# Kernel optimization log

Hardware: AMD Instinct MI355X
Metric: run time of the kernel (lower is better)

Reference implementation:

```python
import jax, jax.numpy as jnp
import numpy as np

TEMP = 0.1
EPS = 1e-12  # torch F.normalize eps


def _normalize(v):
    return v / jnp.maximum(jnp.linalg.norm(v, axis=1, keepdims=True), EPS)


def _scale_loss(a1, a2, b1, c1):
    # diag of exp(a1 @ a2.T / temp): computed directly from paired rows
    # (same math as eye-mask + row-sum in the original).
    diag = jnp.exp(jnp.sum(a1 * a2, axis=1) / TEMP)            # [B]
    denom = (jnp.exp(a1 @ b1.T / TEMP).sum(1, keepdims=True)
             + jnp.exp(a1 @ c1.T / TEMP).sum(1, keepdims=True))  # [B,1]
    # NOTE: [B] / [B,1] broadcasts to [B,B], exactly as in the torch code.
    return jnp.mean(-jnp.log(diag / denom))


def setup_inputs() -> dict:
    key = jax.random.key(0)
    kx, ky, kz = jax.random.split(key, 3)
    shape = (8192, 128)
    return {
        "x": jax.random.normal(kx, shape, dtype=jnp.float32),
        "y": jax.random.normal(ky, shape, dtype=jnp.float32),
        "z": jax.random.normal(kz, shape, dtype=jnp.float32),
    }


def reference(x, y, z):
    x = _normalize(x)
    y = _normalize(y)
    z = _normalize(z)
    B = x.shape[0] // 2
    x1, x2 = x[:B], x[B:]
    y1, y2 = y[:B], y[B:]
    z1, z2 = z[:B], z[B:]

    loss_scale = (_scale_loss(x1, x2, y1, z1)
                  + _scale_loss(y1, y2, x1, z1)
                  + _scale_loss(z1, z2, x1, y1))

    xyz1 = jnp.concatenate([x1, y1, z1], axis=1)  # [B, 3D]
    xyz2 = jnp.concatenate([x2, y2, z2], axis=1)
    m = jnp.exp(xyz1 @ xyz2.T / TEMP)             # [B, B]
    # [B] / [B,1] -> [B,B] broadcast, matching the torch code.
    loss_view = jnp.mean(-jnp.log(jnp.diagonal(m) / m.sum(1, keepdims=True)))

    return loss_view + loss_scale
```

## Files before the change

### kernel.cpp

```cpp
#include <hip/hip_runtime.h>
#include <hip/hip_bf16.h>

#define BHALF 4096
#define DDIM 128
#define KCAT 384
#define TEMP_INV 10.0f
#define EXP2K 14.426950408889634f

typedef __attribute__((ext_vector_type(8))) short short8;
typedef __attribute__((ext_vector_type(4))) float f32x4;

__device__ __forceinline__ void gload16(const ushort* g, ushort* l) {
  __builtin_amdgcn_global_load_lds(
      (const __attribute__((address_space(1))) unsigned int*)g,
      (__attribute__((address_space(3))) unsigned int*)l, 16, 0, 0);
}

__global__ __launch_bounds__(256) void norm_diag_kernel(
    const float* __restrict__ x, const float* __restrict__ y,
    const float* __restrict__ z, ushort* __restrict__ nrm1,
    ushort* __restrict__ nrm2, float* __restrict__ dxyz) {
  int wave = threadIdx.x >> 6;
  int lane = threadIdx.x & 63;
  int gi = blockIdx.x * 4 + wave;
  int mat = gi >> 12;
  int i = gi & 4095;
  const float* src = (mat == 0 ? x : (mat == 1 ? y : z));
  float2 a = *(const float2*)(src + (size_t)i * DDIM + lane * 2);
  float2 b = *(const float2*)(src + (size_t)(i + BHALF) * DDIM + lane * 2);
  float s1 = a.x * a.x + a.y * a.y;
  float s2 = b.x * b.x + b.y * b.y;
  float d = a.x * b.x + a.y * b.y;
#pragma unroll
  for (int m = 1; m < 64; m <<= 1) {
    s1 += __shfl_xor(s1, m, 64);
    s2 += __shfl_xor(s2, m, 64);
    d += __shfl_xor(d, m, 64);
  }
  float r1 = 1.0f / fmaxf(sqrtf(s1), 1e-12f);
  float r2 = 1.0f / fmaxf(sqrtf(s2), 1e-12f);
  ushort* d1 = nrm1 + (size_t)i * KCAT + mat * DDIM + lane * 2;
  ushort* d2 = nrm2 + (size_t)i * KCAT + mat * DDIM + lane * 2;
  __hip_bfloat162 o1, o2;
  o1.x = __float2bfloat16(a.x * r1);
  o1.y = __float2bfloat16(a.y * r1);
  o2.x = __float2bfloat16(b.x * r2);
  o2.y = __float2bfloat16(b.y * r2);
  *(__hip_bfloat162*)d1 = o1;
  *(__hip_bfloat162*)d2 = o2;
  if (lane == 0) dxyz[mat * BHALF + i] = d * r1 * r2;
}


__device__ __forceinline__ void flush_cheap(f32x4 (&acc)[4][4],
                                            float* __restrict__ dst, int base,
                                            int lane) {
#pragma unroll
  for (int m = 0; m < 4; ++m) {
    float s = 0.0f;
#pragma unroll
    for (int n = 0; n < 4; ++n)
#pragma unroll
      for (int r = 0; r < 4; ++r) s += exp2f(acc[m][n][r] * EXP2K);
    s += __shfl_xor(s, 16, 64);
    s += __shfl_xor(s, 32, 64);
    if (lane < 16) atomicAdd(&dst[base + m * 16 + lane], s);
#pragma unroll
    for (int n = 0; n < 4; ++n)
#pragma unroll
      for (int r = 0; r < 4; ++r) acc[m][n][r] = 0.0f;
  }
}

__device__ __forceinline__ void flush_full(f32x4 (&acc)[4][4],
                                           float* __restrict__ rs,
                                           float* __restrict__ cs, int rbase,
                                           int cbase, int lane) {
#pragma unroll
  for (int m = 0; m < 4; ++m)
#pragma unroll
    for (int n = 0; n < 4; ++n)
#pragma unroll
      for (int r = 0; r < 4; ++r)
        acc[m][n][r] = exp2f(acc[m][n][r] * EXP2K);

#pragma unroll
  for (int m = 0; m < 4; ++m) {
    float rsum[4];
#pragma unroll
    for (int r = 0; r < 4; ++r)
      rsum[r] = acc[m][0][r] + acc[m][1][r] + acc[m][2][r] + acc[m][3][r];
#pragma unroll
    for (int r = 0; r < 4; ++r) {
      rsum[r] += __shfl_xor(rsum[r], 1, 64);
      rsum[r] += __shfl_xor(rsum[r], 2, 64);
      rsum[r] += __shfl_xor(rsum[r], 4, 64);
      rsum[r] += __shfl_xor(rsum[r], 8, 64);
    }
    if ((lane & 15) == 0) {
      int rb = rbase + m * 16 + (lane >> 4) * 4;
#pragma unroll
      for (int r = 0; r < 4; ++r) atomicAdd(&rs[rb + r], rsum[r]);
    }
  }

#pragma unroll
  for (int n = 0; n < 4; ++n) {
    float csum = 0.0f;
#pragma unroll
    for (int m = 0; m < 4; ++m)
#pragma unroll
      for (int r = 0; r < 4; ++r) csum += acc[m][n][r];
    csum += __shfl_xor(csum, 16, 64);
    csum += __shfl_xor(csum, 32, 64);
    if (lane < 16) atomicAdd(&cs[cbase + n * 16 + lane], csum);
#pragma unroll
    for (int m = 0; m < 4; ++m)
#pragma unroll
      for (int r = 0; r < 4; ++r) acc[m][n][r] = 0.0f;
  }
}

__global__ __launch_bounds__(512)
__attribute__((amdgpu_waves_per_eu(2))) void gram_fused_kernel(
    const ushort* __restrict__ nrm1, const ushort* __restrict__ nrm2,
    float* __restrict__ sums) {
  __shared__ ushort As[2 * 2 * 256 * 32];
  __shared__ ushort Bs[2 * 2 * 128 * 32];

  int tid = threadIdx.x;
  int lane = tid & 63;
  int wave = tid >> 6;
  int wr = wave >> 1;
  int wc = wave & 1;

  int rowbase = blockIdx.x * 256;
  int colbase = blockIdx.y * 128;

  int srow = lane >> 2;
  int swz8 = ((lane & 3) ^ ((lane >> 3) & 3)) << 3;
  const ushort* gA =
      nrm1 + (size_t)(rowbase + wave * 32 + srow) * KCAT + swz8;
  const ushort* gB1 =
      nrm1 + (size_t)(colbase + wave * 16 + srow) * KCAT + swz8;
  const ushort* gB2 =
      nrm2 + (size_t)(colbase + wave * 16 + srow) * KCAT + swz8;

  int rsel = lane & 15;
  int slot8 = (((lane >> 4) ^ ((rsel >> 1) & 3)) << 3);

  f32x4 acc[4][4] = {};

#define SCHED(t, ao, bp)                                                    \
  do {                                                                      \
    if ((t) < 6)       { ao = (t) * 64;            bp = gB2 + (t) * 64; }   \
    else if ((t) < 8)  { ao = ((t)-6) * 64;        bp = gB1 + 128 + ((t)-6) * 64; } \
    else if ((t) < 10) { ao = ((t)-8) * 64;        bp = gB1 + 256 + ((t)-8) * 64; } \
    else               { ao = 128 + ((t)-10) * 64; bp = gB1 + 256 + ((t)-10) * 64; } \
  } while (0)

#define STAGE(b, ao, bp)                                                    \
  do {                                                                      \
    _Pragma("unroll") for (int ld = 0; ld < 4; ++ld)                        \
      gload16(gA + (ao) + (size_t)(ld & 1) * 16 * KCAT + (ld >> 1) * 32,    \
              &As[(b) * 16384 + (ld >> 1) * 8192 + wave * 1024 +            \
                  (ld & 1) * 512]);                                         \
    _Pragma("unroll") for (int ld = 0; ld < 2; ++ld)                        \
      gload16((bp) + ld * 32,                                               \
              &Bs[(b) * 8192 + ld * 4096 + wave * 512]);                    \
  } while (0)

  {
    int ao; const ushort* bp;
    SCHED(0, ao, bp);
    STAGE(0, ao, bp);
  }

  int buf = 0;
  for (int gt = 0; gt < 12; ++gt) {
    if (gt < 11) {
      int ao; const ushort* bp;
      SCHED(gt + 1, ao, bp);
      STAGE(buf ^ 1, ao, bp);
      asm volatile("s_waitcnt vmcnt(6)" ::: "memory");
    } else {
      asm volatile("s_waitcnt vmcnt(0)" ::: "memory");
    }
    __builtin_amdgcn_s_barrier();
    __builtin_amdgcn_sched_barrier(0);

    const ushort* A = &As[buf * 16384];
    const ushort* B = &Bs[buf * 8192];
    bool g3 = (gt < 6);
#pragma unroll
    for (int kk = 0; kk < 2; ++kk) {
      short8 af[4], bf[4];
#pragma unroll
      for (int m = 0; m < 4; ++m)
        af[m] = *(const short8*)&A[kk * 8192 +
                                   (wr * 64 + m * 16 + rsel) * 32 + slot8];
#pragma unroll
      for (int n = 0; n < 4; ++n)
        bf[n] = *(const short8*)&B[kk * 4096 +
                                   (wc * 64 + n * 16 + rsel) * 32 + slot8];
      if (g3) {
#pragma unroll
        for (int m = 0; m < 4; ++m)
#pragma unroll
          for (int n = 0; n < 4; ++n)
            acc[m][n] = __builtin_amdgcn_mfma_f32_16x16x32_bf16(
                bf[n], af[m], acc[m][n], 0, 0, 0);
      } else {
#pragma unroll
        for (int m = 0; m < 4; ++m)
#pragma unroll
          for (int n = 0; n < 4; ++n)
            acc[m][n] = __builtin_amdgcn_mfma_f32_16x16x32_bf16(
                af[m], bf[n], acc[m][n], 0, 0, 0);
      }
    }
    __builtin_amdgcn_s_barrier();

    if (gt == 5) {
      flush_cheap(acc, sums + 6 * 4096, rowbase + wr * 64, lane);
    } else if (gt == 7) {
      flush_full(acc, sums, sums + 4096, rowbase + wr * 64,
                 colbase + wc * 64, lane);
    } else if (gt == 9) {
      flush_full(acc, sums + 2 * 4096, sums + 3 * 4096, rowbase + wr * 64,
                 colbase + wc * 64, lane);
    }
    buf ^= 1;
  }
  flush_full(acc, sums + 4 * 4096, sums + 5 * 4096, rowbase + wr * 64,
             colbase + wc * 64, lane);
#undef STAGE
#undef SCHED
}

__global__ __launch_bounds__(1024) void loss_kernel(
    const float* __restrict__ sums, const float* __restrict__ dxyz,
    float* __restrict__ out) {
  const float* rs0 = sums;
  const float* cs0 = sums + 4096;
  const float* rs1 = sums + 2 * 4096;
  const float* cs1 = sums + 3 * 4096;
  const float* rs2 = sums + 4 * 4096;
  const float* cs2 = sums + 5 * 4096;
  const float* rs3 = sums + 6 * 4096;
  int tid = threadIdx.x;
  float acc = 0.0f;
  for (int i = tid; i < BHALF; i += 1024) {
    float dxv = dxyz[i];
    float dyv = dxyz[4096 + i];
    float dzv = dxyz[2 * 4096 + i];
    float lx = logf(rs0[i] + rs1[i]) - TEMP_INV * dxv;
    float ly = logf(cs0[i] + rs2[i]) - TEMP_INV * dyv;
    float lz = logf(cs1[i] + cs2[i]) - TEMP_INV * dzv;
    float lv = logf(rs3[i]) - TEMP_INV * (dxv + dyv + dzv);
    acc += lx + ly + lz + lv;
  }
  __shared__ float red[16];
#pragma unroll
  for (int m = 1; m < 64; m <<= 1) acc += __shfl_xor(acc, m, 64);
  if ((tid & 63) == 0) red[tid >> 6] = acc;
  __syncthreads();
  if (tid == 0) {
    float t = 0.0f;
#pragma unroll
    for (int i = 0; i < 16; ++i) t += red[i];
    out[0] = t * (1.0f / 4096.0f);
  }
}

extern "C" void kernel_launch(void* const* d_in, const int* in_sizes, int n_in,
                              void* d_out, int out_size, void* d_ws,
                              size_t ws_size, hipStream_t stream) {
  const float* x = (const float*)d_in[0];
  const float* y = (const float*)d_in[1];
  const float* z = (const float*)d_in[2];
  char* ws = (char*)d_ws;
  ushort* nrm1 = (ushort*)ws;
  ushort* nrm2 = nrm1 + (size_t)BHALF * KCAT;
  float* sums = (float*)(ws + 2 * (size_t)BHALF * KCAT * sizeof(ushort));
  float* dxyz = sums + 7 * 4096;

  hipMemsetAsync(sums, 0, 7 * 4096 * sizeof(float), stream);
  norm_diag_kernel<<<3 * BHALF / 4, 256, 0, stream>>>(x, y, z, nrm1, nrm2,
                                                      dxyz);
  gram_fused_kernel<<<dim3(16, 32), 512, 0, stream>>>(nrm1, nrm2, sums);
  loss_kernel<<<1, 1024, 0, stream>>>(sums, dxyz, (float*)d_out);
}
```

Before: 83.94 us.

## Split fused gram kernel into per-group slab blocks over a 3D grid

```diff
diff --git a/kernel.cpp b/kernel.cpp
--- a/kernel.cpp
+++ b/kernel.cpp
@@ -65,10 +65,6 @@
     s += __shfl_xor(s, 16, 64);
     s += __shfl_xor(s, 32, 64);
     if (lane < 16) atomicAdd(&dst[base + m * 16 + lane], s);
-#pragma unroll
-    for (int n = 0; n < 4; ++n)
-#pragma unroll
-      for (int r = 0; r < 4; ++r) acc[m][n][r] = 0.0f;
   }
 }
 
@@ -114,103 +110,102 @@
     csum += __shfl_xor(csum, 16, 64);
     csum += __shfl_xor(csum, 32, 64);
     if (lane < 16) atomicAdd(&cs[cbase + n * 16 + lane], csum);
-#pragma unroll
-    for (int m = 0; m < 4; ++m)
-#pragma unroll
-      for (int r = 0; r < 4; ++r) acc[m][n][r] = 0.0f;
-  }
-}
-
-__global__ __launch_bounds__(512)
-__attribute__((amdgpu_waves_per_eu(2))) void gram_fused_kernel(
+  }
+}
+
+__global__ __launch_bounds__(256) void gram_slab_kernel(
     const ushort* __restrict__ nrm1, const ushort* __restrict__ nrm2,
     float* __restrict__ sums) {
-  __shared__ ushort As[2 * 2 * 256 * 32];
-  __shared__ ushort Bs[2 * 2 * 128 * 32];
+  __shared__ ushort As[4][128][32];
+  __shared__ ushort Bs[4][128][32];
 
   int tid = threadIdx.x;
   int lane = tid & 63;
   int wave = tid >> 6;
   int wr = wave >> 1;
   int wc = wave & 1;
-
-  int rowbase = blockIdx.x * 256;
+  int g = (blockIdx.z == 0) ? 3 : (int)blockIdx.z - 1;
+  int rowbase = blockIdx.x * 128;
   int colbase = blockIdx.y * 128;
 
+  const ushort* Ab;
+  const ushort* Bb;
+  int nslab;
+  float* rs;
+  float* cs;
+  if (g == 3) {
+    Ab = nrm1;       Bb = nrm2;       nslab = 3;
+    rs = sums + 6 * 4096; cs = nullptr;
+  } else if (g == 0) {
+    Ab = nrm1;       Bb = nrm1 + 128; nslab = 1;
+    rs = sums;            cs = sums + 4096;
+  } else if (g == 1) {
+    Ab = nrm1;       Bb = nrm1 + 256; nslab = 1;
+    rs = sums + 2 * 4096; cs = sums + 3 * 4096;
+  } else {
+    Ab = nrm1 + 128; Bb = nrm1 + 256; nslab = 1;
+    rs = sums + 4 * 4096; cs = sums + 5 * 4096;
+  }
+
   int srow = lane >> 2;
-  int swz8 = ((lane & 3) ^ ((lane >> 3) & 3)) << 3;
+  int schunk = ((lane & 3) ^ ((lane >> 3) & 3)) << 3;
   const ushort* gA =
-      nrm1 + (size_t)(rowbase + wave * 32 + srow) * KCAT + swz8;
-  const ushort* gB1 =
-      nrm1 + (size_t)(colbase + wave * 16 + srow) * KCAT + swz8;
-  const ushort* gB2 =
-      nrm2 + (size_t)(colbase + wave * 16 + srow) * KCAT + swz8;
+      Ab + (size_t)(rowbase + wave * 32 + srow) * KCAT + schunk;
+  const ushort* gB =
+      Bb + (size_t)(colbase + wave * 32 + srow) * KCAT + schunk;
 
   int rsel = lane & 15;
   int slot8 = (((lane >> 4) ^ ((rsel >> 1) & 3)) << 3);
 
   f32x4 acc[4][4] = {};
 
-#define SCHED(t, ao, bp)                                                    \
-  do {                                                                      \
-    if ((t) < 6)       { ao = (t) * 64;            bp = gB2 + (t) * 64; }   \
-    else if ((t) < 8)  { ao = ((t)-6) * 64;        bp = gB1 + 128 + ((t)-6) * 64; } \
-    else if ((t) < 10) { ao = ((t)-8) * 64;        bp = gB1 + 256 + ((t)-8) * 64; } \
-    else               { ao = 128 + ((t)-10) * 64; bp = gB1 + 256 + ((t)-10) * 64; } \
-  } while (0)
-
-#define STAGE(b, ao, bp)                                                    \
-  do {                                                                      \
-    _Pragma("unroll") for (int ld = 0; ld < 4; ++ld)                        \
-      gload16(gA + (ao) + (size_t)(ld & 1) * 16 * KCAT + (ld >> 1) * 32,    \
-              &As[(b) * 16384 + (ld >> 1) * 8192 + wave * 1024 +            \
-                  (ld & 1) * 512]);                                         \
-    _Pragma("unroll") for (int ld = 0; ld < 2; ++ld)                        \
-      gload16((bp) + ld * 32,                                               \
-              &Bs[(b) * 8192 + ld * 4096 + wave * 512]);                    \
-  } while (0)
-
-  {
-    int ao; const ushort* bp;
-    SCHED(0, ao, bp);
-    STAGE(0, ao, bp);
-  }
-
-  int buf = 0;
-  for (int gt = 0; gt < 12; ++gt) {
-    if (gt < 11) {
-      int ao; const ushort* bp;
-      SCHED(gt + 1, ao, bp);
-      STAGE(buf ^ 1, ao, bp);
-      asm volatile("s_waitcnt vmcnt(6)" ::: "memory");
-    } else {
-      asm volatile("s_waitcnt vmcnt(0)" ::: "memory");
-    }
+  for (int slab = 0; slab < nslab; ++slab) {
+    if (slab) {
+      __builtin_amdgcn_s_barrier();
+      __builtin_amdgcn_sched_barrier(0);
+    }
+    int k0 = slab * 128;
+#pragma unroll
+    for (int s = 0; s < 4; ++s) {
+#pragma unroll
+      for (int rg = 0; rg < 2; ++rg) {
+        gload16(gA + k0 + s * 32 + (size_t)rg * 16 * KCAT,
+                &As[s][wave * 32 + rg * 16][0]);
+        gload16(gB + k0 + s * 32 + (size_t)rg * 16 * KCAT,
+                &Bs[s][wave * 32 + rg * 16][0]);
+      }
+    }
+    asm volatile("s_waitcnt vmcnt(0)" ::: "memory");
     __builtin_amdgcn_s_barrier();
     __builtin_amdgcn_sched_barrier(0);
 
-    const ushort* A = &As[buf * 16384];
-    const ushort* B = &Bs[buf * 8192];
-    bool g3 = (gt < 6);
-#pragma unroll
-    for (int kk = 0; kk < 2; ++kk) {
-      short8 af[4], bf[4];
-#pragma unroll
-      for (int m = 0; m < 4; ++m)
-        af[m] = *(const short8*)&A[kk * 8192 +
-                                   (wr * 64 + m * 16 + rsel) * 32 + slot8];
-#pragma unroll
-      for (int n = 0; n < 4; ++n)
-        bf[n] = *(const short8*)&B[kk * 4096 +
-                                   (wc * 64 + n * 16 + rsel) * 32 + slot8];
-      if (g3) {
+    if (g == 3) {
+#pragma unroll
+      for (int kk = 0; kk < 4; ++kk) {
+        short8 af[4], bf[4];
+#pragma unroll
+        for (int m = 0; m < 4; ++m)
+          af[m] = *(const short8*)&As[kk][wr * 64 + m * 16 + rsel][slot8];
+#pragma unroll
+        for (int n = 0; n < 4; ++n)
+          bf[n] = *(const short8*)&Bs[kk][wc * 64 + n * 16 + rsel][slot8];
 #pragma unroll
         for (int m = 0; m < 4; ++m)
 #pragma unroll
           for (int n = 0; n < 4; ++n)
             acc[m][n] = __builtin_amdgcn_mfma_f32_16x16x32_bf16(
                 bf[n], af[m], acc[m][n], 0, 0, 0);
-      } else {
+      }
+    } else {
+#pragma unroll
+      for (int kk = 0; kk < 4; ++kk) {
+        short8 af[4], bf[4];
+#pragma unroll
+        for (int m = 0; m < 4; ++m)
+          af[m] = *(const short8*)&As[kk][wr * 64 + m * 16 + rsel][slot8];
+#pragma unroll
+        for (int n = 0; n < 4; ++n)
+          bf[n] = *(const short8*)&Bs[kk][wc * 64 + n * 16 + rsel][slot8];
 #pragma unroll
         for (int m = 0; m < 4; ++m)
 #pragma unroll
@@ -219,23 +214,12 @@
                 af[m], bf[n], acc[m][n], 0, 0, 0);
       }
     }
-    __builtin_amdgcn_s_barrier();
-
-    if (gt == 5) {
-      flush_cheap(acc, sums + 6 * 4096, rowbase + wr * 64, lane);
-    } else if (gt == 7) {
-      flush_full(acc, sums, sums + 4096, rowbase + wr * 64,
-                 colbase + wc * 64, lane);
-    } else if (gt == 9) {
-      flush_full(acc, sums + 2 * 4096, sums + 3 * 4096, rowbase + wr * 64,
-                 colbase + wc * 64, lane);
-    }
-    buf ^= 1;
-  }
-  flush_full(acc, sums + 4 * 4096, sums + 5 * 4096, rowbase + wr * 64,
-             colbase + wc * 64, lane);
-#undef STAGE
-#undef SCHED
+  }
+
+  if (g == 3)
+    flush_cheap(acc, rs, rowbase + wr * 64, lane);
+  else
+    flush_full(acc, rs, cs, rowbase + wr * 64, colbase + wc * 64, lane);
 }
 
 __global__ __launch_bounds__(1024) void loss_kernel(
@@ -288,6 +272,6 @@
   hipMemsetAsync(sums, 0, 7 * 4096 * sizeof(float), stream);
   norm_diag_kernel<<<3 * BHALF / 4, 256, 0, stream>>>(x, y, z, nrm1, nrm2,
                                                       dxyz);
-  gram_fused_kernel<<<dim3(16, 32), 512, 0, stream>>>(nrm1, nrm2, sums);
+  gram_slab_kernel<<<dim3(32, 32, 4), 256, 0, stream>>>(nrm1, nrm2, sums);
   loss_kernel<<<1, 1024, 0, stream>>>(sums, dxyz, (float*)d_out);
 }
```

Result: faster. 76.95 us (-8.3%).
